# Optimization experiments

Measured on AMD Instinct MI355X. Metric: run time of the kernel, lower is better.

## Reference

```python
import jax, jax.numpy as jnp
import numpy as np

N = 50000      # nodes
E = 625000     # edges
D = 128        # in/hidden channels (equal, required by skip connection)
L = 64         # latent dim
NLAYER = 3
EPS = 1e-5     # batchnorm eps
SLOPE = 0.01   # leaky_relu default negative slope


def setup_inputs() -> dict:
    key = jax.random.key(0)
    ks = jax.random.split(key, 8)
    s = 1.0 / np.sqrt(D)
    x = jax.random.normal(ks[0], (N, D), dtype=jnp.float32)
    edge_index = jax.random.randint(ks[1], (2, E), 0, N, dtype=jnp.int64)
    Ws = jax.random.normal(ks[2], (NLAYER, D, D), dtype=jnp.float32) * s
    bs = jnp.zeros((NLAYER, D), dtype=jnp.float32)
    Wmu = jax.random.normal(ks[3], (D, L), dtype=jnp.float32) * s
    bmu = jnp.zeros((L,), dtype=jnp.float32)
    Wlv = jax.random.normal(ks[4], (D, L), dtype=jnp.float32) * s
    blv = jnp.zeros((L,), dtype=jnp.float32)
    gamma = jnp.ones((D,), dtype=jnp.float32)
    beta = jnp.zeros((D,), dtype=jnp.float32)
    return dict(x=x, edge_index=edge_index, Ws=Ws, bs=bs, Wmu=Wmu, bmu=bmu,
                Wlv=Wlv, blv=blv, gamma=gamma, beta=beta)


def reference(x, edge_index, Ws, bs, Wmu, bmu, Wlv, blv, gamma, beta):
    n = x.shape[0]
    self_idx = jnp.arange(n, dtype=edge_index.dtype)
    src = jnp.concatenate([edge_index[0], self_idx])  # [E+N] with self-loops
    dst = jnp.concatenate([edge_index[1], self_idx])
    # symmetric GCN normalization: deg counted on destination (incl. self-loops)
    deg = jax.ops.segment_sum(jnp.ones(src.shape[0], dtype=x.dtype), dst, num_segments=n)
    dinv = jax.lax.rsqrt(jnp.maximum(deg, 1e-12))  # deg >= 1 thanks to self-loops
    norm = dinv[src] * dinv[dst]                   # [E+N]

    def gcn(h, W, b):
        h = h @ W                                  # transform then propagate (PyG GCNConv)
        msg = h[src] * norm[:, None]               # gather + per-edge scale
        return jax.ops.segment_sum(msg, dst, num_segments=n) + b

    for i in range(NLAYER):
        x_res = x
        x = gcn(x, Ws[i], bs[i])
        # BatchNorm (training mode: batch statistics, biased variance)
        mean = jnp.mean(x, axis=0)
        var = jnp.var(x, axis=0)
        x = (x - mean) * jax.lax.rsqrt(var + EPS) * gamma + beta
        x = jnp.where(x >= 0, x, SLOPE * x)        # leaky_relu
        x = x + x_res                              # skip connection

    mu = gcn(x, Wmu, bmu)
    logvar = gcn(x, Wlv, blv)
    return (mu, logvar)
```

## Files before the change

### kernel.cpp

```cpp
#include <hip/hip_runtime.h>

typedef unsigned int uint;
typedef unsigned short ushort;

#define EPS 1e-5f
#define SLOPE 0.01f
#define GATHER_BLOCKS 2048
#define PK 136

static inline int cdiv(long a, int b) { return (int)((a + b - 1) / b); }

typedef __attribute__((ext_vector_type(8))) short short8;
typedef __attribute__((ext_vector_type(4))) float f32x4;

__device__ inline float bf_lo(uint v) { return __uint_as_float(v << 16); }
__device__ inline float bf_hi(uint v) { return __uint_as_float(v & 0xffff0000u); }
__device__ inline ushort f2bf(float f) {
  uint u = __float_as_uint(f);
  u += 0x7fffu + ((u >> 16) & 1u);
  return (ushort)(u >> 16);
}
__device__ inline uint pack2bf(float a, float b) {
  return (uint)f2bf(a) | ((uint)f2bf(b) << 16);
}

__global__ void deg_kernel(const int* __restrict__ dst, int* __restrict__ degi, int E) {
  int e = blockIdx.x * 256 + threadIdx.x;
  if (e < E) atomicAdd(&degi[dst[e]], 1);
}

__global__ void dinv_kernel(const int* __restrict__ degi, float* __restrict__ dinv, int n) {
  int v = blockIdx.x * 256 + threadIdx.x;
  if (v < n) dinv[v] = rsqrtf((float)(degi[v] + 1));
}

__global__ __launch_bounds__(256) void bsum_kernel(const int* __restrict__ degi,
    int* __restrict__ bsum, int n) {
  int tid = threadIdx.x;
  int i = blockIdx.x * 256 + tid;
  int v = (i < n) ? degi[i] : 0;
  #pragma unroll
  for (int ofs = 32; ofs; ofs >>= 1) v += __shfl_down(v, ofs, 64);
  __shared__ int ws[4];
  if ((tid & 63) == 0) ws[tid >> 6] = v;
  __syncthreads();
  if (tid == 0) bsum[blockIdx.x] = ws[0] + ws[1] + ws[2] + ws[3];
}

__global__ __launch_bounds__(256) void bscan_kernel(const int* __restrict__ bsum,
    int* __restrict__ bofs, int* __restrict__ ptr_end, int nb) {
  int tid = threadIdx.x, lane = tid & 63, wv = tid >> 6;
  __shared__ int wsum[4];
  __shared__ int carry_s, tot_s;
  if (tid == 0) carry_s = 0;
  __syncthreads();
  for (int base = 0; base < nb; base += 256) {
    int i = base + tid;
    int v = (i < nb) ? bsum[i] : 0;
    int inc = v;
    #pragma unroll
    for (int ofs = 1; ofs < 64; ofs <<= 1) {
      int t = __shfl_up(inc, ofs, 64);
      if (lane >= ofs) inc += t;
    }
    if (lane == 63) wsum[wv] = inc;
    __syncthreads();
    if (tid == 0) {
      int a = carry_s;
      for (int w = 0; w < 4; ++w) { int t = wsum[w]; wsum[w] = a; a += t; }
      tot_s = a;
    }
    __syncthreads();
    if (i < nb) bofs[i] = wsum[wv] + inc - v;
    __syncthreads();
    if (tid == 0) carry_s = tot_s;
    __syncthreads();
  }
  if (tid == 0) *ptr_end = carry_s;
}

__global__ __launch_bounds__(256) void ptr_kernel(const int* __restrict__ degi,
    const int* __restrict__ bofs, int* __restrict__ ptr, int n) {
  int tid = threadIdx.x, lane = tid & 63, wv = tid >> 6;
  int i = blockIdx.x * 256 + tid;
  int v = (i < n) ? degi[i] : 0;
  int inc = v;
  #pragma unroll
  for (int ofs = 1; ofs < 64; ofs <<= 1) {
    int t = __shfl_up(inc, ofs, 64);
    if (lane >= ofs) inc += t;
  }
  __shared__ int wsum[4], woff[4];
  if (lane == 63) wsum[wv] = inc;
  __syncthreads();
  if (tid == 0) {
    int a = 0;
    for (int w = 0; w < 4; ++w) { woff[w] = a; a += wsum[w]; }
  }
  __syncthreads();
  if (i < n) ptr[i] = bofs[blockIdx.x] + woff[wv] + inc - v;
}

__global__ void fill_kernel(const int* __restrict__ src, const int* __restrict__ dst,
    const float* __restrict__ dinv, const int* __restrict__ ptr,
    int* __restrict__ fillc, int2* __restrict__ csr, int E) {
  int e = blockIdx.x * 256 + threadIdx.x;
  if (e >= E) return;
  int s = src[e], d = dst[e];
  int pos = ptr[d] + atomicAdd(&fillc[d], 1);
  float c = dinv[s] * dinv[d];
  csr[pos] = make_int2(s, __float_as_int(c));
}

template<bool FUSED, bool WRITEX, bool TWOW>
__global__ __launch_bounds__(256) void mfma_gemm(
    const float* __restrict__ Af, const uint* __restrict__ Az,
    const float* __restrict__ scale, const float* __restrict__ shift,
    const float* __restrict__ xres, float* __restrict__ xout,
    const float* __restrict__ W0, const float* __restrict__ W1,
    ushort* __restrict__ Cbf, int n) {
  __shared__ ushort sWt[128 * PK];
  const int tid = threadIdx.x;
  for (int t = tid; t < 1024; t += 256) {
    const int tk = t & 31;
    const int tc = t >> 5;
    float4 r0, r1, r2, r3;
    if (TWOW) {
      int c = tc * 4;
      const float* Wb = (c < 64) ? W0 : W1;
      int cc = (c < 64) ? c : c - 64;
      r0 = *(const float4*)&Wb[(tk * 4 + 0) * 64 + cc];
      r1 = *(const float4*)&Wb[(tk * 4 + 1) * 64 + cc];
      r2 = *(const float4*)&Wb[(tk * 4 + 2) * 64 + cc];
      r3 = *(const float4*)&Wb[(tk * 4 + 3) * 64 + cc];
    } else {
      r0 = *(const float4*)&W0[(tk * 4 + 0) * 128 + tc * 4];
      r1 = *(const float4*)&W0[(tk * 4 + 1) * 128 + tc * 4];
      r2 = *(const float4*)&W0[(tk * 4 + 2) * 128 + tc * 4];
      r3 = *(const float4*)&W0[(tk * 4 + 3) * 128 + tc * 4];
    }
    const float* p0 = (const float*)&r0;
    const float* p1 = (const float*)&r1;
    const float* p2 = (const float*)&r2;
    const float* p3 = (const float*)&r3;
    #pragma unroll
    for (int j = 0; j < 4; ++j) {
      uint lo = (uint)f2bf(p0[j]) | ((uint)f2bf(p1[j]) << 16);
      uint hi = (uint)f2bf(p2[j]) | ((uint)f2bf(p3[j]) << 16);
      *(uint2*)&sWt[(tc * 4 + j) * PK + tk * 4] = make_uint2(lo, hi);
    }
  }
  __syncthreads();

  const int w = tid >> 6;
  const int lane = tid & 63;
  const int l16 = lane & 15, q = lane >> 4;
  const int row0 = blockIdx.x * 128 + w * 32;

  f32x4 acc[2][8];
  #pragma unroll
  for (int mt = 0; mt < 2; ++mt)
    #pragma unroll
    for (int nt = 0; nt < 8; ++nt)
      acc[mt][nt] = (f32x4){0.f, 0.f, 0.f, 0.f};

  for (int ks = 0; ks < 4; ++ks) {
    const int kbase = ks * 32 + q * 8;
    short8 afrag[2];
    #pragma unroll
    for (int mt = 0; mt < 2; ++mt) {
      int row = row0 + mt * 16 + l16;
      float av[8] = {0.f,0.f,0.f,0.f,0.f,0.f,0.f,0.f};
      if (row < n) {
        if constexpr (FUSED) {
          uint4 zw = *(const uint4*)&Az[(size_t)row * 64 + (kbase >> 1)];
          float zv[8] = { bf_lo(zw.x), bf_hi(zw.x), bf_lo(zw.y), bf_hi(zw.y),
                          bf_lo(zw.z), bf_hi(zw.z), bf_lo(zw.w), bf_hi(zw.w) };
          float4 sc0 = *(const float4*)&scale[kbase];
          float4 sc1 = *(const float4*)&scale[kbase + 4];
          float4 sh0 = *(const float4*)&shift[kbase];
          float4 sh1 = *(const float4*)&shift[kbase + 4];
          const float* scp = (const float*)&sc0;
          float scv[8] = { sc0.x, sc0.y, sc0.z, sc0.w, sc1.x, sc1.y, sc1.z, sc1.w };
          float shv[8] = { sh0.x, sh0.y, sh0.z, sh0.w, sh1.x, sh1.y, sh1.z, sh1.w };
          const float* Xr = xres + (size_t)row * 128 + kbase;
          float4 x0 = *(const float4*)&Xr[0];
          float4 x1 = *(const float4*)&Xr[4];
          float xv[8] = { x0.x, x0.y, x0.z, x0.w, x1.x, x1.y, x1.z, x1.w };
          (void)scp;
          #pragma unroll
          for (int j = 0; j < 8; ++j) {
            float u = fmaf(zv[j], scv[j], shv[j]);
            u = u >= 0.f ? u : SLOPE * u;
            av[j] = u + xv[j];
          }
          if constexpr (WRITEX) {
            float* Xo = xout + (size_t)row * 128 + kbase;
            *(float4*)&Xo[0] = make_float4(av[0], av[1], av[2], av[3]);
            *(float4*)&Xo[4] = make_float4(av[4], av[5], av[6], av[7]);
          }
        } else {
          const float* Ar = Af + (size_t)row * 128 + kbase;
          float4 a0 = *(const float4*)&Ar[0];
          float4 a1 = *(const float4*)&Ar[4];
          av[0]=a0.x; av[1]=a0.y; av[2]=a0.z; av[3]=a0.w;
          av[4]=a1.x; av[5]=a1.y; av[6]=a1.z; av[7]=a1.w;
        }
      }
      short8 af;
      #pragma unroll
      for (int j = 0; j < 8; ++j) af[j] = (short)f2bf(av[j]);
      afrag[mt] = af;
    }
    #pragma unroll
    for (int nt = 0; nt < 8; ++nt) {
      short8 bfrag = *(const short8*)&sWt[(nt * 16 + l16) * PK + kbase];
      acc[0][nt] = __builtin_amdgcn_mfma_f32_16x16x32_bf16(afrag[0], bfrag, acc[0][nt], 0, 0, 0);
      acc[1][nt] = __builtin_amdgcn_mfma_f32_16x16x32_bf16(afrag[1], bfrag, acc[1][nt], 0, 0, 0);
    }
  }
  #pragma unroll
  for (int mt = 0; mt < 2; ++mt) {
    int rbase = row0 + mt * 16 + q * 4;
    #pragma unroll
    for (int nt = 0; nt < 8; ++nt) {
      int col = nt * 16 + l16;
      #pragma unroll
      for (int r = 0; r < 4; ++r) {
        int row = rbase + r;
        if (row < n) Cbf[(size_t)row * 128 + col] = f2bf(acc[mt][nt][r]);
      }
    }
  }
}

__global__ __launch_bounds__(256) void gather_layer(const int* __restrict__ ptr,
    const int2* __restrict__ csr, const uint* __restrict__ ybf,
    const float* __restrict__ b, const float* __restrict__ dinv,
    uint* __restrict__ zbf, float* __restrict__ psum, float* __restrict__ psq, int n) {
  const int tid = threadIdx.x;
  const int lane = tid & 63, wv = tid >> 6;
  float2 bb = *(const float2*)&b[lane * 2];
  float sx = 0.f, sy = 0.f, qx = 0.f, qy = 0.f;
  const int wstride = gridDim.x * 4;
  for (int w = blockIdx.x * 4 + wv; w < n; w += wstride) {
    float dv = dinv[w], c0 = dv * dv;
    uint yv = ybf[(size_t)w * 64 + lane];
    float ax = fmaf(c0, bf_lo(yv), bb.x);
    float ay = fmaf(c0, bf_hi(yv), bb.y);
    int j = ptr[w], end = ptr[w + 1];
    if ((j & 1) && j < end) {
      int2 e = csr[j];
      uint v = ybf[(size_t)e.x * 64 + lane];
      float c = __int_as_float(e.y);
      ax = fmaf(c, bf_lo(v), ax); ay = fmaf(c, bf_hi(v), ay);
      ++j;
    }
    for (; j + 3 < end; j += 4) {
      int4 p0 = *(const int4*)&csr[j];
      int4 p1 = *(const int4*)&csr[j + 2];
      uint v0 = ybf[(size_t)p0.x * 64 + lane];
      uint v1 = ybf[(size_t)p0.z * 64 + lane];
      uint v2 = ybf[(size_t)p1.x * 64 + lane];
      uint v3 = ybf[(size_t)p1.z * 64 + lane];
      float c0_ = __int_as_float(p0.y), c1_ = __int_as_float(p0.w);
      float c2_ = __int_as_float(p1.y), c3_ = __int_as_float(p1.w);
      ax = fmaf(c0_, bf_lo(v0), ax); ay = fmaf(c0_, bf_hi(v0), ay);
      ax = fmaf(c1_, bf_lo(v1), ax); ay = fmaf(c1_, bf_hi(v1), ay);
      ax = fmaf(c2_, bf_lo(v2), ax); ay = fmaf(c2_, bf_hi(v2), ay);
      ax = fmaf(c3_, bf_lo(v3), ax); ay = fmaf(c3_, bf_hi(v3), ay);
    }
    for (; j < end; ++j) {
      int2 e = csr[j];
      uint v = ybf[(size_t)e.x * 64 + lane];
      float c = __int_as_float(e.y);
      ax = fmaf(c, bf_lo(v), ax); ay = fmaf(c, bf_hi(v), ay);
    }
    zbf[(size_t)w * 64 + lane] = pack2bf(ax, ay);
    sx += ax; sy += ay;
    qx = fmaf(ax, ax, qx); qy = fmaf(ay, ay, qy);
  }
  __shared__ float red[4][64];
  red[wv][lane] = sx; __syncthreads();
  if (wv == 0) psum[(size_t)blockIdx.x * 128 + lane * 2] =
      red[0][lane] + red[1][lane] + red[2][lane] + red[3][lane];
  __syncthreads();
  red[wv][lane] = sy; __syncthreads();
  if (wv == 0) psum[(size_t)blockIdx.x * 128 + lane * 2 + 1] =
      red[0][lane] + red[1][lane] + red[2][lane] + red[3][lane];
  __syncthreads();
  red[wv][lane] = qx; __syncthreads();
  if (wv == 0) psq[(size_t)blockIdx.x * 128 + lane * 2] =
      red[0][lane] + red[1][lane] + red[2][lane] + red[3][lane];
  __syncthreads();
  red[wv][lane] = qy; __syncthreads();
  if (wv == 0) psq[(size_t)blockIdx.x * 128 + lane * 2 + 1] =
      red[0][lane] + red[1][lane] + red[2][lane] + red[3][lane];
}

__global__ __launch_bounds__(256) void gather_heads(const int* __restrict__ ptr,
    const int2* __restrict__ csr, const uint* __restrict__ ybf,
    const float* __restrict__ bmu, const float* __restrict__ blv,
    const float* __restrict__ dinv, float* __restrict__ out, int n) {
  int w = (blockIdx.x * 256 + threadIdx.x) >> 6;
  if (w >= n) return;
  int lane = threadIdx.x & 63;
  int col = lane * 2;
  float* obase; const float* bias; int cc;
  if (col < 64) { obase = out; bias = bmu; cc = col; }
  else { obase = out + (size_t)n * 64; bias = blv; cc = col - 64; }
  float dv = dinv[w], c0 = dv * dv;
  uint yv = ybf[(size_t)w * 64 + lane];
  float ax = fmaf(c0, bf_lo(yv), bias[cc]);
  float ay = fmaf(c0, bf_hi(yv), bias[cc + 1]);
  int j = ptr[w], end = ptr[w + 1];
  if ((j & 1) && j < end) {
    int2 e = csr[j];
    uint v = ybf[(size_t)e.x * 64 + lane];
    float c = __int_as_float(e.y);
    ax = fmaf(c, bf_lo(v), ax); ay = fmaf(c, bf_hi(v), ay);
    ++j;
  }
  for (; j + 3 < end; j += 4) {
    int4 p0 = *(const int4*)&csr[j];
    int4 p1 = *(const int4*)&csr[j + 2];
    uint v0 = ybf[(size_t)p0.x * 64 + lane];
    uint v1 = ybf[(size_t)p0.z * 64 + lane];
    uint v2 = ybf[(size_t)p1.x * 64 + lane];
    uint v3 = ybf[(size_t)p1.z * 64 + lane];
    float c0_ = __int_as_float(p0.y), c1_ = __int_as_float(p0.w);
    float c2_ = __int_as_float(p1.y), c3_ = __int_as_float(p1.w);
    ax = fmaf(c0_, bf_lo(v0), ax); ay = fmaf(c0_, bf_hi(v0), ay);
    ax = fmaf(c1_, bf_lo(v1), ax); ay = fmaf(c1_, bf_hi(v1), ay);
    ax = fmaf(c2_, bf_lo(v2), ax); ay = fmaf(c2_, bf_hi(v2), ay);
    ax = fmaf(c3_, bf_lo(v3), ax); ay = fmaf(c3_, bf_hi(v3), ay);
  }
  for (; j < end; ++j) {
    int2 e = csr[j];
    uint v = ybf[(size_t)e.x * 64 + lane];
    float c = __int_as_float(e.y);
    ax = fmaf(c, bf_lo(v), ax); ay = fmaf(c, bf_hi(v), ay);
  }
  *(float2*)&obase[(size_t)w * 64 + cc] = make_float2(ax, ay);
}

__global__ __launch_bounds__(256) void bnfin_kernel(const float* __restrict__ psum,
    const float* __restrict__ psq, const float* __restrict__ gamma,
    const float* __restrict__ beta, float* __restrict__ scale,
    float* __restrict__ shift, int n, int nb) {
  const int c = blockIdx.x;
  const int tid = threadIdx.x;
  float s = 0.f, s2 = 0.f;
  for (int b = tid; b < nb; b += 256) {
    s += psum[(size_t)b * 128 + c];
    s2 += psq[(size_t)b * 128 + c];
  }
  #pragma unroll
  for (int ofs = 32; ofs; ofs >>= 1) {
    s += __shfl_down(s, ofs, 64);
    s2 += __shfl_down(s2, ofs, 64);
  }
  __shared__ float ws[4], wq[4];
  if ((tid & 63) == 0) { ws[tid >> 6] = s; wq[tid >> 6] = s2; }
  __syncthreads();
  if (tid == 0) {
    float S = ws[0] + ws[1] + ws[2] + ws[3];
    float Q = wq[0] + wq[1] + wq[2] + wq[3];
    float mean = S / (float)n;
    float var = Q / (float)n - mean * mean;
    float inv = rsqrtf(var + EPS);
    float sc = gamma[c] * inv;
    scale[c] = sc;
    shift[c] = beta[c] - mean * sc;
  }
}

extern "C" void kernel_launch(void* const* d_in, const int* in_sizes, int n_in,
                              void* d_out, int out_size, void* d_ws, size_t ws_size,
                              hipStream_t stream) {
  const float* x     = (const float*)d_in[0];
  const int*   ei    = (const int*)d_in[1];
  const float* Ws    = (const float*)d_in[2];
  const float* bs    = (const float*)d_in[3];
  const float* Wmu   = (const float*)d_in[4];
  const float* bmu   = (const float*)d_in[5];
  const float* Wlv   = (const float*)d_in[6];
  const float* blv   = (const float*)d_in[7];
  const float* gamma = (const float*)d_in[8];
  const float* beta  = (const float*)d_in[9];
  float* out = (float*)d_out;

  const int n = in_sizes[0] / 128;
  const int E = in_sizes[1] / 2;
  const int* srcI = ei;
  const int* dstI = ei + E;
  const int nb = cdiv(n, 256);

  char* wsp = (char*)d_ws;
  size_t off = 0;
  auto alloc = [&](size_t bytes) -> void* {
    void* p = wsp + off;
    off += (bytes + 255) & ~(size_t)255;
    return p;
  };
  int*    degi  = (int*)alloc((size_t)n * 4);
  float*  dinv  = (float*)alloc((size_t)n * 4);
  int*    ptr   = (int*)alloc((size_t)(n + 1) * 4);
  int*    fillc = (int*)alloc((size_t)n * 4);
  int*    bsum  = (int*)alloc((size_t)nb * 4);
  int*    bofs  = (int*)alloc((size_t)nb * 4);
  int2*   csr   = (int2*)alloc((size_t)E * 8);
  ushort* ybf   = (ushort*)alloc((size_t)n * 128 * 2);
  uint*   zbf   = (uint*)alloc((size_t)n * 64 * 4);
  float*  xbuf  = (float*)alloc((size_t)n * 128 * 4);
  float*  psum  = (float*)alloc((size_t)GATHER_BLOCKS * 128 * 4);
  float*  psq   = (float*)alloc((size_t)GATHER_BLOCKS * 128 * 4);
  float*  scale = (float*)alloc(128 * 4);
  float*  shift = (float*)alloc(128 * 4);
  (void)n_in; (void)out_size; (void)ws_size;

  hipMemsetAsync(degi, 0, (size_t)n * 4, stream);
  hipMemsetAsync(fillc, 0, (size_t)n * 4, stream);
  deg_kernel<<<cdiv(E, 256), 256, 0, stream>>>(dstI, degi, E);
  dinv_kernel<<<cdiv(n, 256), 256, 0, stream>>>(degi, dinv, n);
  bsum_kernel<<<nb, 256, 0, stream>>>(degi, bsum, n);
  bscan_kernel<<<1, 256, 0, stream>>>(bsum, bofs, ptr + n, nb);
  ptr_kernel<<<nb, 256, 0, stream>>>(degi, bofs, ptr, n);
  fill_kernel<<<cdiv(E, 256), 256, 0, stream>>>(srcI, dstI, dinv, ptr, fillc, csr, E);

  const int ggrid = cdiv(n, 128);
  const int wgrid = cdiv((long)n * 64, 256);

  mfma_gemm<false, false, false><<<ggrid, 256, 0, stream>>>(
      x, nullptr, nullptr, nullptr, nullptr, nullptr, Ws, nullptr, ybf, n);
  gather_layer<<<GATHER_BLOCKS, 256, 0, stream>>>(ptr, csr, (const uint*)ybf, bs, dinv, zbf, psum, psq, n);
  bnfin_kernel<<<128, 256, 0, stream>>>(psum, psq, gamma, beta, scale, shift, n, GATHER_BLOCKS);
  mfma_gemm<true, true, false><<<ggrid, 256, 0, stream>>>(
      nullptr, zbf, scale, shift, x, xbuf, Ws + 16384, nullptr, ybf, n);
  gather_layer<<<GATHER_BLOCKS, 256, 0, stream>>>(ptr, csr, (const uint*)ybf, bs + 128, dinv, zbf, psum, psq, n);
  bnfin_kernel<<<128, 256, 0, stream>>>(psum, psq, gamma, beta, scale, shift, n, GATHER_BLOCKS);
  mfma_gemm<true, true, false><<<ggrid, 256, 0, stream>>>(
      nullptr, zbf, scale, shift, xbuf, xbuf, Ws + 32768, nullptr, ybf, n);
  gather_layer<<<GATHER_BLOCKS, 256, 0, stream>>>(ptr, csr, (const uint*)ybf, bs + 256, dinv, zbf, psum, psq, n);
  bnfin_kernel<<<128, 256, 0, stream>>>(psum, psq, gamma, beta, scale, shift, n, GATHER_BLOCKS);
  mfma_gemm<true, false, true><<<ggrid, 256, 0, stream>>>(
      nullptr, zbf, scale, shift, xbuf, nullptr, Wmu, Wlv, ybf, n);
  gather_heads<<<wgrid, 256, 0, stream>>>(ptr, csr, (const uint*)ybf, bmu, blv, dinv, out, n);
}
```

Before: 301.3 us.

## Compress CSR to 32-bit entries, bf16 residual, two-node gather per wave

Packs each CSR entry into 32 bits: a 16-bit source index and a bf16 edge coefficient. The residual activations are now stored in bf16 instead of fp32. Gather kernels process two destination nodes per wave so more independent loads are in flight, and gather_heads becomes a grid-stride kernel. dinv is folded into bsum and the two memsets are merged. The changes cut memory traffic and launches, but they assume fewer than 65536 nodes and reduce precision of the skip connection and the edge norms.

```diff
diff --git a/kernel.cpp b/kernel.cpp
--- a/kernel.cpp
+++ b/kernel.cpp
@@ -29,20 +29,17 @@
   if (e < E) atomicAdd(&degi[dst[e]], 1);
 }
 
-__global__ void dinv_kernel(const int* __restrict__ degi, float* __restrict__ dinv, int n) {
-  int v = blockIdx.x * 256 + threadIdx.x;
-  if (v < n) dinv[v] = rsqrtf((float)(degi[v] + 1));
-}
-
 __global__ __launch_bounds__(256) void bsum_kernel(const int* __restrict__ degi,
-    int* __restrict__ bsum, int n) {
+    int* __restrict__ bsum, float* __restrict__ dinv, int n) {
   int tid = threadIdx.x;
   int i = blockIdx.x * 256 + tid;
   int v = (i < n) ? degi[i] : 0;
+  if (i < n) dinv[i] = rsqrtf((float)(v + 1));
+  int r = v;
   #pragma unroll
-  for (int ofs = 32; ofs; ofs >>= 1) v += __shfl_down(v, ofs, 64);
+  for (int ofs = 32; ofs; ofs >>= 1) r += __shfl_down(r, ofs, 64);
   __shared__ int ws[4];
-  if ((tid & 63) == 0) ws[tid >> 6] = v;
+  if ((tid & 63) == 0) ws[tid >> 6] = r;
   __syncthreads();
   if (tid == 0) bsum[blockIdx.x] = ws[0] + ws[1] + ws[2] + ws[3];
 }
@@ -103,20 +100,21 @@
 
 __global__ void fill_kernel(const int* __restrict__ src, const int* __restrict__ dst,
     const float* __restrict__ dinv, const int* __restrict__ ptr,
-    int* __restrict__ fillc, int2* __restrict__ csr, int E) {
+    int* __restrict__ fillc, uint* __restrict__ csr, int E) {
   int e = blockIdx.x * 256 + threadIdx.x;
   if (e >= E) return;
   int s = src[e], d = dst[e];
   int pos = ptr[d] + atomicAdd(&fillc[d], 1);
   float c = dinv[s] * dinv[d];
-  csr[pos] = make_int2(s, __float_as_int(c));
-}
-
-template<bool FUSED, bool WRITEX, bool TWOW>
+  csr[pos] = (uint)s | ((uint)f2bf(c) << 16);
+}
+
+template<bool FUSED, bool WRITEX, bool TWOW, bool XRESBF>
 __global__ __launch_bounds__(256) void mfma_gemm(
     const float* __restrict__ Af, const uint* __restrict__ Az,
     const float* __restrict__ scale, const float* __restrict__ shift,
-    const float* __restrict__ xres, float* __restrict__ xout,
+    const float* __restrict__ xresf, const uint* __restrict__ xresb,
+    uint* __restrict__ xoutb,
     const float* __restrict__ W0, const float* __restrict__ W1,
     ushort* __restrict__ Cbf, int n) {
   __shared__ ushort sWt[128 * PK];
@@ -180,14 +178,20 @@
           float4 sc1 = *(const float4*)&scale[kbase + 4];
           float4 sh0 = *(const float4*)&shift[kbase];
           float4 sh1 = *(const float4*)&shift[kbase + 4];
-          const float* scp = (const float*)&sc0;
           float scv[8] = { sc0.x, sc0.y, sc0.z, sc0.w, sc1.x, sc1.y, sc1.z, sc1.w };
           float shv[8] = { sh0.x, sh0.y, sh0.z, sh0.w, sh1.x, sh1.y, sh1.z, sh1.w };
-          const float* Xr = xres + (size_t)row * 128 + kbase;
-          float4 x0 = *(const float4*)&Xr[0];
-          float4 x1 = *(const float4*)&Xr[4];
-          float xv[8] = { x0.x, x0.y, x0.z, x0.w, x1.x, x1.y, x1.z, x1.w };
-          (void)scp;
+          float xv[8];
+          if constexpr (XRESBF) {
+            uint4 xw = *(const uint4*)&xresb[(size_t)row * 64 + (kbase >> 1)];
+            xv[0]=bf_lo(xw.x); xv[1]=bf_hi(xw.x); xv[2]=bf_lo(xw.y); xv[3]=bf_hi(xw.y);
+            xv[4]=bf_lo(xw.z); xv[5]=bf_hi(xw.z); xv[6]=bf_lo(xw.w); xv[7]=bf_hi(xw.w);
+          } else {
+            const float* Xr = xresf + (size_t)row * 128 + kbase;
+            float4 x0 = *(const float4*)&Xr[0];
+            float4 x1 = *(const float4*)&Xr[4];
+            xv[0]=x0.x; xv[1]=x0.y; xv[2]=x0.z; xv[3]=x0.w;
+            xv[4]=x1.x; xv[5]=x1.y; xv[6]=x1.z; xv[7]=x1.w;
+          }
           #pragma unroll
           for (int j = 0; j < 8; ++j) {
             float u = fmaf(zv[j], scv[j], shv[j]);
@@ -195,9 +199,10 @@
             av[j] = u + xv[j];
           }
           if constexpr (WRITEX) {
-            float* Xo = xout + (size_t)row * 128 + kbase;
-            *(float4*)&Xo[0] = make_float4(av[0], av[1], av[2], av[3]);
-            *(float4*)&Xo[4] = make_float4(av[4], av[5], av[6], av[7]);
+            uint4 o;
+            o.x = pack2bf(av[0], av[1]); o.y = pack2bf(av[2], av[3]);
+            o.z = pack2bf(av[4], av[5]); o.w = pack2bf(av[6], av[7]);
+            *(uint4*)&xoutb[(size_t)row * 64 + (kbase >> 1)] = o;
           }
         } else {
           const float* Ar = Af + (size_t)row * 128 + kbase;
@@ -234,51 +239,89 @@
   }
 }
 
+#define EDGE_FMA(E_, R_, AX_, AY_) { float c_ = bf_hi(E_); \
+  AX_ = fmaf(c_, bf_lo(R_), AX_); AY_ = fmaf(c_, bf_hi(R_), AY_); }
+
 __global__ __launch_bounds__(256) void gather_layer(const int* __restrict__ ptr,
-    const int2* __restrict__ csr, const uint* __restrict__ ybf,
+    const uint* __restrict__ csr, const uint* __restrict__ ybf,
     const float* __restrict__ b, const float* __restrict__ dinv,
     uint* __restrict__ zbf, float* __restrict__ psum, float* __restrict__ psq, int n) {
   const int tid = threadIdx.x;
   const int lane = tid & 63, wv = tid >> 6;
   float2 bb = *(const float2*)&b[lane * 2];
   float sx = 0.f, sy = 0.f, qx = 0.f, qy = 0.f;
-  const int wstride = gridDim.x * 4;
-  for (int w = blockIdx.x * 4 + wv; w < n; w += wstride) {
-    float dv = dinv[w], c0 = dv * dv;
-    uint yv = ybf[(size_t)w * 64 + lane];
-    float ax = fmaf(c0, bf_lo(yv), bb.x);
-    float ay = fmaf(c0, bf_hi(yv), bb.y);
-    int j = ptr[w], end = ptr[w + 1];
-    if ((j & 1) && j < end) {
-      int2 e = csr[j];
-      uint v = ybf[(size_t)e.x * 64 + lane];
-      float c = __int_as_float(e.y);
-      ax = fmaf(c, bf_lo(v), ax); ay = fmaf(c, bf_hi(v), ay);
-      ++j;
-    }
-    for (; j + 3 < end; j += 4) {
-      int4 p0 = *(const int4*)&csr[j];
-      int4 p1 = *(const int4*)&csr[j + 2];
-      uint v0 = ybf[(size_t)p0.x * 64 + lane];
-      uint v1 = ybf[(size_t)p0.z * 64 + lane];
-      uint v2 = ybf[(size_t)p1.x * 64 + lane];
-      uint v3 = ybf[(size_t)p1.z * 64 + lane];
-      float c0_ = __int_as_float(p0.y), c1_ = __int_as_float(p0.w);
-      float c2_ = __int_as_float(p1.y), c3_ = __int_as_float(p1.w);
-      ax = fmaf(c0_, bf_lo(v0), ax); ay = fmaf(c0_, bf_hi(v0), ay);
-      ax = fmaf(c1_, bf_lo(v1), ax); ay = fmaf(c1_, bf_hi(v1), ay);
-      ax = fmaf(c2_, bf_lo(v2), ax); ay = fmaf(c2_, bf_hi(v2), ay);
-      ax = fmaf(c3_, bf_lo(v3), ax); ay = fmaf(c3_, bf_hi(v3), ay);
-    }
-    for (; j < end; ++j) {
-      int2 e = csr[j];
-      uint v = ybf[(size_t)e.x * 64 + lane];
-      float c = __int_as_float(e.y);
-      ax = fmaf(c, bf_lo(v), ax); ay = fmaf(c, bf_hi(v), ay);
-    }
-    zbf[(size_t)w * 64 + lane] = pack2bf(ax, ay);
-    sx += ax; sy += ay;
-    qx = fmaf(ax, ax, qx); qy = fmaf(ay, ay, qy);
+  const int stride = gridDim.x * 8;
+  for (int w = (blockIdx.x * 4 + wv) * 2; w < n; w += stride) {
+    const bool has1 = (w + 1) < n;
+    int p0 = ptr[w], p1 = ptr[w + 1];
+    int p2 = has1 ? ptr[w + 2] : p1;
+    float dv0 = dinv[w], c00 = dv0 * dv0;
+    uint y0 = ybf[(size_t)w * 64 + lane];
+    float a0x = fmaf(c00, bf_lo(y0), bb.x);
+    float a0y = fmaf(c00, bf_hi(y0), bb.y);
+    float a1x = 0.f, a1y = 0.f;
+    if (has1) {
+      float dv1 = dinv[w + 1], c01 = dv1 * dv1;
+      uint y1 = ybf[(size_t)(w + 1) * 64 + lane];
+      a1x = fmaf(c01, bf_lo(y1), bb.x);
+      a1y = fmaf(c01, bf_hi(y1), bb.y);
+    }
+    int j0 = p0, j1 = p1;
+    while (j0 + 4 <= p1 && j1 + 4 <= p2) {
+      uint e0 = csr[j0], e1 = csr[j0+1], e2 = csr[j0+2], e3 = csr[j0+3];
+      uint f0 = csr[j1], f1 = csr[j1+1], f2 = csr[j1+2], f3 = csr[j1+3];
+      uint r0 = ybf[(size_t)(e0 & 0xffffu) * 64 + lane];
+      uint r1 = ybf[(size_t)(e1 & 0xffffu) * 64 + lane];
+      uint r2 = ybf[(size_t)(e2 & 0xffffu) * 64 + lane];
+      uint r3 = ybf[(size_t)(e3 & 0xffffu) * 64 + lane];
+      uint s0 = ybf[(size_t)(f0 & 0xffffu) * 64 + lane];
+      uint s1 = ybf[(size_t)(f1 & 0xffffu) * 64 + lane];
+      uint s2 = ybf[(size_t)(f2 & 0xffffu) * 64 + lane];
+      uint s3 = ybf[(size_t)(f3 & 0xffffu) * 64 + lane];
+      EDGE_FMA(e0, r0, a0x, a0y); EDGE_FMA(e1, r1, a0x, a0y);
+      EDGE_FMA(e2, r2, a0x, a0y); EDGE_FMA(e3, r3, a0x, a0y);
+      EDGE_FMA(f0, s0, a1x, a1y); EDGE_FMA(f1, s1, a1x, a1y);
+      EDGE_FMA(f2, s2, a1x, a1y); EDGE_FMA(f3, s3, a1x, a1y);
+      j0 += 4; j1 += 4;
+    }
+    while (j0 + 4 <= p1) {
+      uint e0 = csr[j0], e1 = csr[j0+1], e2 = csr[j0+2], e3 = csr[j0+3];
+      uint r0 = ybf[(size_t)(e0 & 0xffffu) * 64 + lane];
+      uint r1 = ybf[(size_t)(e1 & 0xffffu) * 64 + lane];
+      uint r2 = ybf[(size_t)(e2 & 0xffffu) * 64 + lane];
+      uint r3 = ybf[(size_t)(e3 & 0xffffu) * 64 + lane];
+      EDGE_FMA(e0, r0, a0x, a0y); EDGE_FMA(e1, r1, a0x, a0y);
+      EDGE_FMA(e2, r2, a0x, a0y); EDGE_FMA(e3, r3, a0x, a0y);
+      j0 += 4;
+    }
+    for (; j0 < p1; ++j0) {
+      uint e = csr[j0];
+      uint r = ybf[(size_t)(e & 0xffffu) * 64 + lane];
+      EDGE_FMA(e, r, a0x, a0y);
+    }
+    while (j1 + 4 <= p2) {
+      uint f0 = csr[j1], f1 = csr[j1+1], f2 = csr[j1+2], f3 = csr[j1+3];
+      uint s0 = ybf[(size_t)(f0 & 0xffffu) * 64 + lane];
+      uint s1 = ybf[(size_t)(f1 & 0xffffu) * 64 + lane];
+      uint s2 = ybf[(size_t)(f2 & 0xffffu) * 64 + lane];
+      uint s3 = ybf[(size_t)(f3 & 0xffffu) * 64 + lane];
+      EDGE_FMA(f0, s0, a1x, a1y); EDGE_FMA(f1, s1, a1x, a1y);
+      EDGE_FMA(f2, s2, a1x, a1y); EDGE_FMA(f3, s3, a1x, a1y);
+      j1 += 4;
+    }
+    for (; j1 < p2; ++j1) {
+      uint f = csr[j1];
+      uint s = ybf[(size_t)(f & 0xffffu) * 64 + lane];
+      EDGE_FMA(f, s, a1x, a1y);
+    }
+    zbf[(size_t)w * 64 + lane] = pack2bf(a0x, a0y);
+    sx += a0x; sy += a0y;
+    qx = fmaf(a0x, a0x, qx); qy = fmaf(a0y, a0y, qy);
+    if (has1) {
+      zbf[(size_t)(w + 1) * 64 + lane] = pack2bf(a1x, a1y);
+      sx += a1x; sy += a1y;
+      qx = fmaf(a1x, a1x, qx); qy = fmaf(a1y, a1y, qy);
+    }
   }
   __shared__ float red[4][64];
   red[wv][lane] = sx; __syncthreads();
@@ -299,49 +342,84 @@
 }
 
 __global__ __launch_bounds__(256) void gather_heads(const int* __restrict__ ptr,
-    const int2* __restrict__ csr, const uint* __restrict__ ybf,
+    const uint* __restrict__ csr, const uint* __restrict__ ybf,
     const float* __restrict__ bmu, const float* __restrict__ blv,
     const float* __restrict__ dinv, float* __restrict__ out, int n) {
-  int w = (blockIdx.x * 256 + threadIdx.x) >> 6;
-  if (w >= n) return;
-  int lane = threadIdx.x & 63;
+  const int tid = threadIdx.x;
+  const int lane = tid & 63, wv = tid >> 6;
   int col = lane * 2;
-  float* obase; const float* bias; int cc;
-  if (col < 64) { obase = out; bias = bmu; cc = col; }
-  else { obase = out + (size_t)n * 64; bias = blv; cc = col - 64; }
-  float dv = dinv[w], c0 = dv * dv;
-  uint yv = ybf[(size_t)w * 64 + lane];
-  float ax = fmaf(c0, bf_lo(yv), bias[cc]);
-  float ay = fmaf(c0, bf_hi(yv), bias[cc + 1]);
-  int j = ptr[w], end = ptr[w + 1];
-  if ((j & 1) && j < end) {
-    int2 e = csr[j];
-    uint v = ybf[(size_t)e.x * 64 + lane];
-    float c = __int_as_float(e.y);
-    ax = fmaf(c, bf_lo(v), ax); ay = fmaf(c, bf_hi(v), ay);
-    ++j;
-  }
-  for (; j + 3 < end; j += 4) {
-    int4 p0 = *(const int4*)&csr[j];
-    int4 p1 = *(const int4*)&csr[j + 2];
-    uint v0 = ybf[(size_t)p0.x * 64 + lane];
-    uint v1 = ybf[(size_t)p0.z * 64 + lane];
-    uint v2 = ybf[(size_t)p1.x * 64 + lane];
-    uint v3 = ybf[(size_t)p1.z * 64 + lane];
-    float c0_ = __int_as_float(p0.y), c1_ = __int_as_float(p0.w);
-    float c2_ = __int_as_float(p1.y), c3_ = __int_as_float(p1.w);
-    ax = fmaf(c0_, bf_lo(v0), ax); ay = fmaf(c0_, bf_hi(v0), ay);
-    ax = fmaf(c1_, bf_lo(v1), ax); ay = fmaf(c1_, bf_hi(v1), ay);
-    ax = fmaf(c2_, bf_lo(v2), ax); ay = fmaf(c2_, bf_hi(v2), ay);
-    ax = fmaf(c3_, bf_lo(v3), ax); ay = fmaf(c3_, bf_hi(v3), ay);
-  }
-  for (; j < end; ++j) {
-    int2 e = csr[j];
-    uint v = ybf[(size_t)e.x * 64 + lane];
-    float c = __int_as_float(e.y);
-    ax = fmaf(c, bf_lo(v), ax); ay = fmaf(c, bf_hi(v), ay);
-  }
-  *(float2*)&obase[(size_t)w * 64 + cc] = make_float2(ax, ay);
+  const float* bias; size_t obase; int cc;
+  if (col < 64) { obase = 0; bias = bmu; cc = col; }
+  else { obase = (size_t)n * 64; bias = blv; cc = col - 64; }
+  float bx = bias[cc], by = bias[cc + 1];
+  const int stride = gridDim.x * 8;
+  for (int w = (blockIdx.x * 4 + wv) * 2; w < n; w += stride) {
+    const bool has1 = (w + 1) < n;
+    int p0 = ptr[w], p1 = ptr[w + 1];
+    int p2 = has1 ? ptr[w + 2] : p1;
+    float dv0 = dinv[w], c00 = dv0 * dv0;
+    uint y0 = ybf[(size_t)w * 64 + lane];
+    float a0x = fmaf(c00, bf_lo(y0), bx);
+    float a0y = fmaf(c00, bf_hi(y0), by);
+    float a1x = 0.f, a1y = 0.f;
+    if (has1) {
+      float dv1 = dinv[w + 1], c01 = dv1 * dv1;
+      uint y1 = ybf[(size_t)(w + 1) * 64 + lane];
+      a1x = fmaf(c01, bf_lo(y1), bx);
+      a1y = fmaf(c01, bf_hi(y1), by);
+    }
+    int j0 = p0, j1 = p1;
+    while (j0 + 4 <= p1 && j1 + 4 <= p2) {
+      uint e0 = csr[j0], e1 = csr[j0+1], e2 = csr[j0+2], e3 = csr[j0+3];
+      uint f0 = csr[j1], f1 = csr[j1+1], f2 = csr[j1+2], f3 = csr[j1+3];
+      uint r0 = ybf[(size_t)(e0 & 0xffffu) * 64 + lane];
+      uint r1 = ybf[(size_t)(e1 & 0xffffu) * 64 + lane];
+      uint r2 = ybf[(size_t)(e2 & 0xffffu) * 64 + lane];
+      uint r3 = ybf[(size_t)(e3 & 0xffffu) * 64 + lane];
+      uint s0 = ybf[(size_t)(f0 & 0xffffu) * 64 + lane];
+      uint s1 = ybf[(size_t)(f1 & 0xffffu) * 64 + lane];
+      uint s2 = ybf[(size_t)(f2 & 0xffffu) * 64 + lane];
+      uint s3 = ybf[(size_t)(f3 & 0xffffu) * 64 + lane];
+      EDGE_FMA(e0, r0, a0x, a0y); EDGE_FMA(e1, r1, a0x, a0y);
+      EDGE_FMA(e2, r2, a0x, a0y); EDGE_FMA(e3, r3, a0x, a0y);
+      EDGE_FMA(f0, s0, a1x, a1y); EDGE_FMA(f1, s1, a1x, a1y);
+      EDGE_FMA(f2, s2, a1x, a1y); EDGE_FMA(f3, s3, a1x, a1y);
+      j0 += 4; j1 += 4;
+    }
+    while (j0 + 4 <= p1) {
+      uint e0 = csr[j0], e1 = csr[j0+1], e2 = csr[j0+2], e3 = csr[j0+3];
+      uint r0 = ybf[(size_t)(e0 & 0xffffu) * 64 + lane];
+      uint r1 = ybf[(size_t)(e1 & 0xffffu) * 64 + lane];
+      uint r2 = ybf[(size_t)(e2 & 0xffffu) * 64 + lane];
+      uint r3 = ybf[(size_t)(e3 & 0xffffu) * 64 + lane];
+      EDGE_FMA(e0, r0, a0x, a0y); EDGE_FMA(e1, r1, a0x, a0y);
+      EDGE_FMA(e2, r2, a0x, a0y); EDGE_FMA(e3, r3, a0x, a0y);
+      j0 += 4;
+    }
+    for (; j0 < p1; ++j0) {
+      uint e = csr[j0];
+      uint r = ybf[(size_t)(e & 0xffffu) * 64 + lane];
+      EDGE_FMA(e, r, a0x, a0y);
+    }
+    while (j1 + 4 <= p2) {
+      uint f0 = csr[j1], f1 = csr[j1+1], f2 = csr[j1+2], f3 = csr[j1+3];
+      uint s0 = ybf[(size_t)(f0 & 0xffffu) * 64 + lane];
+      uint s1 = ybf[(size_t)(f1 & 0xffffu) * 64 + lane];
+      uint s2 = ybf[(size_t)(f2 & 0xffffu) * 64 + lane];
+      uint s3 = ybf[(size_t)(f3 & 0xffffu) * 64 + lane];
+      EDGE_FMA(f0, s0, a1x, a1y); EDGE_FMA(f1, s1, a1x, a1y);
+      EDGE_FMA(f2, s2, a1x, a1y); EDGE_FMA(f3, s3, a1x, a1y);
+      j1 += 4;
+    }
+    for (; j1 < p2; ++j1) {
+      uint f = csr[j1];
+      uint s = ybf[(size_t)(f & 0xffffu) * 64 + lane];
+      EDGE_FMA(f, s, a1x, a1y);
+    }
+    *(float2*)&out[obase + (size_t)w * 64 + cc] = make_float2(a0x, a0y);
+    if (has1)
+      *(float2*)&out[obase + (size_t)(w + 1) * 64 + cc] = make_float2(a1x, a1y);
+  }
 }
 
 __global__ __launch_bounds__(256) void bnfin_kernel(const float* __restrict__ psum,
@@ -403,47 +481,44 @@
     off += (bytes + 255) & ~(size_t)255;
     return p;
   };
-  int*    degi  = (int*)alloc((size_t)n * 4);
+  int*    degi  = (int*)alloc((size_t)2 * n * 4);
+  int*    fillc = degi + n;
   float*  dinv  = (float*)alloc((size_t)n * 4);
   int*    ptr   = (int*)alloc((size_t)(n + 1) * 4);
-  int*    fillc = (int*)alloc((size_t)n * 4);
   int*    bsum  = (int*)alloc((size_t)nb * 4);
   int*    bofs  = (int*)alloc((size_t)nb * 4);
-  int2*   csr   = (int2*)alloc((size_t)E * 8);
+  uint*   csr   = (uint*)alloc((size_t)E * 4);
   ushort* ybf   = (ushort*)alloc((size_t)n * 128 * 2);
   uint*   zbf   = (uint*)alloc((size_t)n * 64 * 4);
-  float*  xbuf  = (float*)alloc((size_t)n * 128 * 4);
+  uint*   xbbf  = (uint*)alloc((size_t)n * 64 * 4);
   float*  psum  = (float*)alloc((size_t)GATHER_BLOCKS * 128 * 4);
   float*  psq   = (float*)alloc((size_t)GATHER_BLOCKS * 128 * 4);
   float*  scale = (float*)alloc(128 * 4);
   float*  shift = (float*)alloc(128 * 4);
   (void)n_in; (void)out_size; (void)ws_size;
 
-  hipMemsetAsync(degi, 0, (size_t)n * 4, stream);
-  hipMemsetAsync(fillc, 0, (size_t)n * 4, stream);
+  hipMemsetAsync(degi, 0, (size_t)2 * n * 4, stream);
   deg_kernel<<<cdiv(E, 256), 256, 0, stream>>>(dstI, degi, E);
-  dinv_kernel<<<cdiv(n, 256), 256, 0, stream>>>(degi, dinv, n);
-  bsum_kernel<<<nb, 256, 0, stream>>>(degi, bsum, n);
+  bsum_kernel<<<nb, 256, 0, stream>>>(degi, bsum, dinv, n);
   bscan_kernel<<<1, 256, 0, stream>>>(bsum, bofs, ptr + n, nb);
   ptr_kernel<<<nb, 256, 0, stream>>>(degi, bofs, ptr, n);
   fill_kernel<<<cdiv(E, 256), 256, 0, stream>>>(srcI, dstI, dinv, ptr, fillc, csr, E);
 
   const int ggrid = cdiv(n, 128);
-  const int wgrid = cdiv((long)n * 64, 256);
-
-  mfma_gemm<false, false, false><<<ggrid, 256, 0, stream>>>(
-      x, nullptr, nullptr, nullptr, nullptr, nullptr, Ws, nullptr, ybf, n);
+
+  mfma_gemm<false, false, false, false><<<ggrid, 256, 0, stream>>>(
+      x, nullptr, nullptr, nullptr, nullptr, nullptr, nullptr, Ws, nullptr, ybf, n);
   gather_layer<<<GATHER_BLOCKS, 256, 0, stream>>>(ptr, csr, (const uint*)ybf, bs, dinv, zbf, psum, psq, n);
   bnfin_kernel<<<128, 256, 0, stream>>>(psum, psq, gamma, beta, scale, shift, n, GATHER_BLOCKS);
-  mfma_gemm<true, true, false><<<ggrid, 256, 0, stream>>>(
-      nullptr, zbf, scale, shift, x, xbuf, Ws + 16384, nullptr, ybf, n);
+  mfma_gemm<true, true, false, false><<<ggrid, 256, 0, stream>>>(
+      nullptr, zbf, scale, shift, x, nullptr, xbbf, Ws + 16384, nullptr, ybf, n);
   gather_layer<<<GATHER_BLOCKS, 256, 0, stream>>>(ptr, csr, (const uint*)ybf, bs + 128, dinv, zbf, psum, psq, n);
   bnfin_kernel<<<128, 256, 0, stream>>>(psum, psq, gamma, beta, scale, shift, n, GATHER_BLOCKS);
-  mfma_gemm<true, true, false><<<ggrid, 256, 0, stream>>>(
-      nullptr, zbf, scale, shift, xbuf, xbuf, Ws + 32768, nullptr, ybf, n);
+  mfma_gemm<true, true, false, true><<<ggrid, 256, 0, stream>>>(
+      nullptr, zbf, scale, shift, nullptr, xbbf, xbbf, Ws + 32768, nullptr, ybf, n);
   gather_layer<<<GATHER_BLOCKS, 256, 0, stream>>>(ptr, csr, (const uint*)ybf, bs + 256, dinv, zbf, psum, psq, n);
   bnfin_kernel<<<128, 256, 0, stream>>>(psum, psq, gamma, beta, scale, shift, n, GATHER_BLOCKS);
-  mfma_gemm<true, false, true><<<ggrid, 256, 0, stream>>>(
-      nullptr, zbf, scale, shift, xbuf, nullptr, Wmu, Wlv, ybf, n);
-  gather_heads<<<wgrid, 256, 0, stream>>>(ptr, csr, (const uint*)ybf, bmu, blv, dinv, out, n);
-}
+  mfma_gemm<true, false, true, true><<<ggrid, 256, 0, stream>>>(
+      nullptr, zbf, scale, shift, nullptr, xbbf, nullptr, Wmu, Wlv, ybf, n);
+  gather_heads<<<GATHER_BLOCKS, 256, 0, stream>>>(ptr, csr, (const uint*)ybf, bmu, blv, dinv, out, n);
+}
```

Result: slower. 309.5 us (+2.7%).
